# Performance work log

Measured on AMD Instinct MI355X. Metric: run time of the kernel, lower is better.

## Reference

```python
import jax, jax.numpy as jnp
import numpy as np

CONTEXT_FRAMES = 10
H = 200  # LSTM hidden size
F = 48   # tactile feature size
A = 6    # action dim


def _lstm_cell(x, h, c, Wih, Whh, bih, bhh):
    # PyTorch gate order: i, f, g, o
    gates = x @ Wih.T + h @ Whh.T + (bih + bhh)
    i, f, g, o = jnp.split(gates, 4, axis=-1)
    i = jax.nn.sigmoid(i)
    f = jax.nn.sigmoid(f)
    g = jnp.tanh(g)
    o = jax.nn.sigmoid(o)
    c = f * c + i * g
    h = o * jnp.tanh(c)
    return h, c


def setup_inputs() -> dict:
    key = jax.random.key(0)
    ks = jax.random.split(key, 16)
    T, B = 120, 4096
    tactiles = jax.random.normal(ks[0], (T, B, F), dtype=jnp.float32)
    actions = jax.random.normal(ks[1], (T, B, A), dtype=jnp.float32)
    s = 1.0 / np.sqrt(H)
    u = lambda k, shp: jax.random.uniform(k, shp, jnp.float32, -s, s)
    return {
        "tactiles": tactiles,
        "actions": actions,
        # lstm1: input 48 -> hidden 200
        "W_ih1": u(ks[2], (4 * H, F)), "W_hh1": u(ks[3], (4 * H, H)),
        "b_ih1": u(ks[4], (4 * H,)), "b_hh1": u(ks[5], (4 * H,)),
        # lstm2: input 248 -> hidden 200
        "W_ih2": u(ks[6], (4 * H, H + F)), "W_hh2": u(ks[7], (4 * H, H)),
        "b_ih2": u(ks[8], (4 * H,)), "b_hh2": u(ks[9], (4 * H,)),
        # fc1: 248 -> 200, fc2: 200 -> 48
        "fc1_w": u(ks[10], (H, H + F)), "fc1_b": u(ks[11], (H,)),
        "fc2_w": u(ks[12], (F, H)), "fc2_b": u(ks[13], (F,)),
    }


def reference(tactiles, actions, W_ih1, W_hh1, b_ih1, b_hh1,
              W_ih2, W_hh2, b_ih2, b_hh2, fc1_w, fc1_b, fc2_w, fc2_b):
    T, B, _ = tactiles.shape
    state = actions[0]  # [B, A]

    def step(carry, xs):
        h1, c1, h2, c2, prev_out4 = carry
        tact_t, act_t, t = xs
        # after the context window, feed back the previous prediction
        inp = jnp.where(t > CONTEXT_FRAMES - 1, prev_out4, tact_t)  # [B, 48]
        h1, c1 = _lstm_cell(inp, h1, c1, W_ih1, W_hh1, b_ih1, b_hh1)
        tiled = jnp.tile(jnp.concatenate([act_t, state], axis=1), (1, 4))  # [B, 48]
        x2 = jnp.concatenate([h1, tiled], axis=1)  # [B, 248]
        h2, c2 = _lstm_cell(x2, h2, c2, W_ih2, W_hh2, b_ih2, b_hh2)
        x3 = jnp.concatenate([h2, inp], axis=1)  # [B, 248]
        out3 = jnp.tanh(x3 @ fc1_w.T + fc1_b)
        out4 = jnp.tanh(out3 @ fc2_w.T + fc2_b)  # [B, 48]
        return (h1, c1, h2, c2, out4), out4

    z = lambda d: jnp.zeros((B, d), dtype=tactiles.dtype)
    carry0 = (z(H), z(H), z(H), z(H), z(F))
    xs = (tactiles[:-1], actions[1:], jnp.arange(T - 1))
    _, out4s = jax.lax.scan(step, carry0, xs)
    # torch code returns [last context out4] + [out4 for index 10..T-2]
    return out4s[CONTEXT_FRAMES - 1:]  # [T - 10, B, 48]
```

## Files before the change

### kernel.cpp

```cpp
#include <hip/hip_runtime.h>
#include <stdint.h>
#include <stddef.h>

#define HDIM 200
#define FDIM 48
#define ADIM 6
#define BTOT 4096
#define NSTEP 119
#define CTXM1 9
#define MROWS 16

typedef __attribute__((ext_vector_type(8))) short short8;
typedef __attribute__((ext_vector_type(4))) float floatx4;

#define OFF_W1P 0u
#define OFF_W2P 425984u
#define OFF_W3P 1171456u
#define OFF_W4P 1277952u
#define OFF_B1  1299456u
#define OFF_B2  1302784u
#define OFF_B3  1306112u
#define OFF_B4  1306944u

__device__ __forceinline__ unsigned short f2bf(float f) {
  unsigned int u = __float_as_uint(f);
  u += 0x7FFFu + ((u >> 16) & 1u);
  return (unsigned short)(u >> 16);
}
__device__ __forceinline__ float sigm(float x) {
  return 1.0f / (1.0f + __expf(-x));
}
__device__ __forceinline__ float tanh_(float x) {
  return 1.0f - 2.0f / (1.0f + __expf(2.0f * x));
}

__global__ void actp_pack(
    const float* __restrict__ Wih1, const float* __restrict__ Whh1,
    const float* __restrict__ bih1, const float* __restrict__ bhh1,
    const float* __restrict__ Wih2, const float* __restrict__ Whh2,
    const float* __restrict__ bih2, const float* __restrict__ bhh2,
    const float* __restrict__ fc1w, const float* __restrict__ fc1b,
    const float* __restrict__ fc2w, const float* __restrict__ fc2b,
    unsigned short* __restrict__ W1p, unsigned short* __restrict__ W2p,
    unsigned short* __restrict__ W3p, unsigned short* __restrict__ W4p,
    float* __restrict__ b1, float* __restrict__ b2,
    float* __restrict__ b3, float* __restrict__ b4) {
  int g = blockIdx.x * blockDim.x + threadIdx.x;
  if (g < 26624) {
    int lane = g & 63, tc = g >> 6;
    int chunk = tc & 7, tile = tc >> 3;
    int p = tile * 16 + (lane & 15);
    int gate = p / 208, u = p - gate * 208;
    int srow = gate * 200 + u;
    int kb = chunk * 32 + (lane >> 4) * 8;
    unsigned short* d = W1p + (size_t)g * 8;
#pragma unroll
    for (int j = 0; j < 8; ++j) {
      int k = kb + j;
      float v = 0.f;
      if (u < 200) {
        if (k < 48) v = Wih1[srow * 48 + k];
        else if (k < 248) v = Whh1[srow * 200 + (k - 48)];
      }
      d[j] = f2bf(v);
    }
  } else if (g < 73216) {
    int g2 = g - 26624;
    int lane = g2 & 63, tc = g2 >> 6;
    int chunk = tc % 14, tile = tc / 14;
    int p = tile * 16 + (lane & 15);
    int gate = p / 208, u = p - gate * 208;
    int srow = gate * 200 + u;
    int kb = chunk * 32 + (lane >> 4) * 8;
    unsigned short* d = W2p + (size_t)g2 * 8;
#pragma unroll
    for (int j = 0; j < 8; ++j) {
      int k = kb + j;
      float v = 0.f;
      if (u < 200) v = (k < 248) ? Wih2[srow * 248 + k] : Whh2[srow * 200 + (k - 248)];
      d[j] = f2bf(v);
    }
  } else if (g < 79872) {
    int g3 = g - 73216;
    int lane = g3 & 63, tc = g3 >> 6;
    int chunk = tc & 7, tile = tc >> 3;
    int p = tile * 16 + (lane & 15);
    int kb = chunk * 32 + (lane >> 4) * 8;
    unsigned short* d = W3p + (size_t)g3 * 8;
#pragma unroll
    for (int j = 0; j < 8; ++j) {
      int k = kb + j;
      float v = (p < 200 && k < 248) ? fc1w[p * 248 + k] : 0.f;
      d[j] = f2bf(v);
    }
  } else if (g < 81216) {
    int g4 = g - 79872;
    int lane = g4 & 63, tc = g4 >> 6;
    int chunk = tc % 7, tile = tc / 7;
    int p = tile * 16 + (lane & 15);
    int kb = chunk * 32 + (lane >> 4) * 8;
    unsigned short* d = W4p + (size_t)g4 * 8;
#pragma unroll
    for (int j = 0; j < 8; ++j) {
      int k = kb + j;
      float v = (k < 200) ? fc2w[p * 200 + k] : 0.f;
      d[j] = f2bf(v);
    }
  } else if (g < 81216 + 1920) {
    int i = g - 81216;
    if (i < 832) {
      int gate = i / 208, u = i - gate * 208;
      b1[i] = (u < 200) ? (bih1[gate * 200 + u] + bhh1[gate * 200 + u]) : 0.f;
    } else if (i < 1664) {
      int p = i - 832;
      int gate = p / 208, u = p - gate * 208;
      b2[p] = (u < 200) ? (bih2[gate * 200 + u] + bhh2[gate * 200 + u]) : 0.f;
    } else if (i < 1872) {
      int p = i - 1664;
      b3[p] = (p < 200) ? fc1b[p] : 0.f;
    } else {
      int p = i - 1872;
      b4[p] = fc2b[p];
    }
  }
}

__global__ __launch_bounds__(512, 2) void actp_main(
    const float* __restrict__ tact,
    const float* __restrict__ acts,
    const unsigned short* __restrict__ W1p, const unsigned short* __restrict__ W2p,
    const unsigned short* __restrict__ W3p, const unsigned short* __restrict__ W4p,
    const float* __restrict__ b1, const float* __restrict__ b2,
    const float* __restrict__ b3, const float* __restrict__ b4,
    float* __restrict__ out)
{
  __shared__ unsigned short x1[2][MROWS][264];
  __shared__ unsigned short x2[2][MROWS][456];
  __shared__ unsigned short x3[MROWS][264];
  __shared__ unsigned short x4[MROWS][232];
  __shared__ float c1s[MROWS][228];
  __shared__ float c2s[MROWS][228];

  const int tid = threadIdx.x;
  const int wv = tid >> 6;
  const int lane = tid & 63;
  const int n16 = lane & 15;
  const int qd = lane >> 4;
  const int row0 = (int)blockIdx.x * MROWS;

  for (int i = tid; i < 2 * MROWS * 264; i += 512) (&x1[0][0][0])[i] = 0;
  for (int i = tid; i < 2 * MROWS * 456; i += 512) (&x2[0][0][0])[i] = 0;
  for (int i = tid; i < MROWS * 264; i += 512) (&x3[0][0])[i] = 0;
  for (int i = tid; i < MROWS * 232; i += 512) (&x4[0][0])[i] = 0;
  for (int i = tid; i < MROWS * 228; i += 512) { (&c1s[0][0])[i] = 0.f; (&c2s[0][0])[i] = 0.f; }
  if (tid < 192) {
    int r = tid / 12, f0 = (tid % 12) * 4;
    const float* src = &tact[((size_t)(row0 + r)) * FDIM + f0];
#pragma unroll
    for (int j = 0; j < 4; ++j) {
      unsigned short v = f2bf(src[j]);
      x1[0][r][f0 + j] = v;
      x3[r][HDIM + f0 + j] = v;
    }
  } else if (tid < 384) {
    int idx = tid - 192;
    int r = idx / 12, a = idx % 12;
    float vf = (a < ADIM) ? acts[((size_t)BTOT + row0 + r) * ADIM + a]
                          : acts[((size_t)(row0 + r)) * ADIM + (a - ADIM)];
    unsigned short v = f2bf(vf);
    unsigned short* d = &x2[0][r][HDIM];
    d[a] = v; d[12 + a] = v; d[24 + a] = v; d[36 + a] = v;
  }
  __syncthreads();

  for (int t = 0; t < NSTEP; ++t) {
    const int cur = t & 1, nxt = cur ^ 1;

    {
      short8 A0[8];
#pragma unroll
      for (int c = 0; c < 8; ++c) A0[c] = *(const short8*)&x1[cur][n16][c * 32 + qd * 8];
      for (int ut = wv; ut < 13; ut += 8) {
        float bi = b1[(0 * 13 + ut) * 16 + n16];
        float bff = b1[(1 * 13 + ut) * 16 + n16];
        float bg = b1[(2 * 13 + ut) * 16 + n16];
        float bo = b1[(3 * 13 + ut) * 16 + n16];
        floatx4 ai = {bi, bi, bi, bi}, af = {bff, bff, bff, bff};
        floatx4 ag = {bg, bg, bg, bg}, ao = {bo, bo, bo, bo};
        const short8* wi = (const short8*)W1p + (size_t)(0 * 13 + ut) * 8 * 64 + lane;
        const short8* wf = (const short8*)W1p + (size_t)(1 * 13 + ut) * 8 * 64 + lane;
        const short8* wg = (const short8*)W1p + (size_t)(2 * 13 + ut) * 8 * 64 + lane;
        const short8* wo = (const short8*)W1p + (size_t)(3 * 13 + ut) * 8 * 64 + lane;
#pragma unroll
        for (int c = 0; c < 8; ++c) {
          ai = __builtin_amdgcn_mfma_f32_16x16x32_bf16(A0[c], wi[c * 64], ai, 0, 0, 0);
          af = __builtin_amdgcn_mfma_f32_16x16x32_bf16(A0[c], wf[c * 64], af, 0, 0, 0);
          ag = __builtin_amdgcn_mfma_f32_16x16x32_bf16(A0[c], wg[c * 64], ag, 0, 0, 0);
          ao = __builtin_amdgcn_mfma_f32_16x16x32_bf16(A0[c], wo[c * 64], ao, 0, 0, 0);
        }
        int u = ut * 16 + n16;
        bool live = (u < HDIM);
#pragma unroll
        for (int r = 0; r < 4; ++r) {
          int m = qd * 4 + r;
          float gi = sigm(ai[r]), gf = sigm(af[r]);
          float gg = tanh_(ag[r]), go = sigm(ao[r]);
          float cp = c1s[m][u];
          float cn = gf * cp + gi * gg;
          float hn = go * tanh_(cn);
          if (live) {
            c1s[m][u] = cn;
            unsigned short hb = f2bf(hn);
            x2[cur][m][u] = hb;
            x1[nxt][m][FDIM + u] = hb;
          }
        }
      }
    }
    __syncthreads();

    {
      short8 A0[14];
#pragma unroll
      for (int c = 0; c < 14; ++c) A0[c] = *(const short8*)&x2[cur][n16][c * 32 + qd * 8];
      for (int ut = wv; ut < 13; ut += 8) {
        float bi = b2[(0 * 13 + ut) * 16 + n16];
        float bff = b2[(1 * 13 + ut) * 16 + n16];
        float bg = b2[(2 * 13 + ut) * 16 + n16];
        float bo = b2[(3 * 13 + ut) * 16 + n16];
        floatx4 ai = {bi, bi, bi, bi}, af = {bff, bff, bff, bff};
        floatx4 ag = {bg, bg, bg, bg}, ao = {bo, bo, bo, bo};
        const short8* wi = (const short8*)W2p + (size_t)(0 * 13 + ut) * 14 * 64 + lane;
        const short8* wf = (const short8*)W2p + (size_t)(1 * 13 + ut) * 14 * 64 + lane;
        const short8* wg = (const short8*)W2p + (size_t)(2 * 13 + ut) * 14 * 64 + lane;
        const short8* wo = (const short8*)W2p + (size_t)(3 * 13 + ut) * 14 * 64 + lane;
#pragma unroll
        for (int c = 0; c < 14; ++c) {
          ai = __builtin_amdgcn_mfma_f32_16x16x32_bf16(A0[c], wi[c * 64], ai, 0, 0, 0);
          af = __builtin_amdgcn_mfma_f32_16x16x32_bf16(A0[c], wf[c * 64], af, 0, 0, 0);
          ag = __builtin_amdgcn_mfma_f32_16x16x32_bf16(A0[c], wg[c * 64], ag, 0, 0, 0);
          ao = __builtin_amdgcn_mfma_f32_16x16x32_bf16(A0[c], wo[c * 64], ao, 0, 0, 0);
        }
        int u = ut * 16 + n16;
        bool live = (u < HDIM);
#pragma unroll
        for (int r = 0; r < 4; ++r) {
          int m = qd * 4 + r;
          float gi = sigm(ai[r]), gf = sigm(af[r]);
          float gg = tanh_(ag[r]), go = sigm(ao[r]);
          float cp = c2s[m][u];
          float cn = gf * cp + gi * gg;
          float hn = go * tanh_(cn);
          if (live) {
            c2s[m][u] = cn;
            unsigned short hb = f2bf(hn);
            x3[m][u] = hb;
            x2[nxt][m][248 + u] = hb;
          }
        }
      }
    }
    __syncthreads();

    if (t >= CTXM1) {
      {
        short8 A0[8];
#pragma unroll
        for (int c = 0; c < 8; ++c) A0[c] = *(const short8*)&x3[n16][c * 32 + qd * 8];
        for (int nt = wv; nt < 13; nt += 8) {
          float bb = b3[nt * 16 + n16];
          floatx4 ac = {bb, bb, bb, bb};
          const short8* wp = (const short8*)W3p + (size_t)nt * 8 * 64 + lane;
#pragma unroll
          for (int c = 0; c < 8; ++c)
            ac = __builtin_amdgcn_mfma_f32_16x16x32_bf16(A0[c], wp[c * 64], ac, 0, 0, 0);
          int col = nt * 16 + n16;
#pragma unroll
          for (int r = 0; r < 4; ++r) x4[qd * 4 + r][col] = f2bf(tanh_(ac[r]));
        }
      }
      __syncthreads();
      if (wv < 3) {
        short8 A0[7];
#pragma unroll
        for (int c = 0; c < 7; ++c) A0[c] = *(const short8*)&x4[n16][c * 32 + qd * 8];
        float bb = b4[wv * 16 + n16];
        floatx4 ac = {bb, bb, bb, bb};
        const short8* wp = (const short8*)W4p + (size_t)wv * 7 * 64 + lane;
#pragma unroll
        for (int c = 0; c < 7; ++c)
          ac = __builtin_amdgcn_mfma_f32_16x16x32_bf16(A0[c], wp[c * 64], ac, 0, 0, 0);
        int col = wv * 16 + n16;
#pragma unroll
        for (int r = 0; r < 4; ++r) {
          int m = qd * 4 + r;
          float of = tanh_(ac[r]);
          out[((size_t)(t - CTXM1) * BTOT + row0 + m) * FDIM + col] = of;
          if (t < NSTEP - 1) {
            unsigned short bv = f2bf(of);
            x1[nxt][m][col] = bv;
            x3[m][HDIM + col] = bv;
          }
        }
      }
    } else {
      if (wv < 3) {
        int idx = wv * 64 + lane;
        int r = idx / 12, f0 = (idx % 12) * 4;
        const float* src = &tact[((size_t)(t + 1) * BTOT + row0 + r) * FDIM + f0];
#pragma unroll
        for (int j = 0; j < 4; ++j) {
          unsigned short v = f2bf(src[j]);
          x1[nxt][r][f0 + j] = v;
          x3[r][HDIM + f0 + j] = v;
        }
      }
    }
    if (wv >= 3 && wv < 6 && t < NSTEP - 1) {
      int idx = (wv - 3) * 64 + lane;
      int r = idx / 12, a = idx % 12;
      float vf = (a < ADIM) ? acts[((size_t)(t + 2) * BTOT + row0 + r) * ADIM + a]
                            : acts[((size_t)(row0 + r)) * ADIM + (a - ADIM)];
      unsigned short v = f2bf(vf);
      unsigned short* d = &x2[nxt][r][HDIM];
      d[a] = v; d[12 + a] = v; d[24 + a] = v; d[36 + a] = v;
    }
    __syncthreads();
  }
}

extern "C" void kernel_launch(void* const* d_in, const int* in_sizes, int n_in,
                              void* d_out, int out_size, void* d_ws, size_t ws_size,
                              hipStream_t stream) {
  const float* tact = (const float*)d_in[0];
  const float* acts = (const float*)d_in[1];
  const float* Wih1 = (const float*)d_in[2];
  const float* Whh1 = (const float*)d_in[3];
  const float* bih1 = (const float*)d_in[4];
  const float* bhh1 = (const float*)d_in[5];
  const float* Wih2 = (const float*)d_in[6];
  const float* Whh2 = (const float*)d_in[7];
  const float* bih2 = (const float*)d_in[8];
  const float* bhh2 = (const float*)d_in[9];
  const float* fc1w = (const float*)d_in[10];
  const float* fc1b = (const float*)d_in[11];
  const float* fc2w = (const float*)d_in[12];
  const float* fc2b = (const float*)d_in[13];

  uint8_t* ws = (uint8_t*)d_ws;
  unsigned short* W1p = (unsigned short*)(ws + OFF_W1P);
  unsigned short* W2p = (unsigned short*)(ws + OFF_W2P);
  unsigned short* W3p = (unsigned short*)(ws + OFF_W3P);
  unsigned short* W4p = (unsigned short*)(ws + OFF_W4P);
  float* b1 = (float*)(ws + OFF_B1);
  float* b2 = (float*)(ws + OFF_B2);
  float* b3 = (float*)(ws + OFF_B3);
  float* b4 = (float*)(ws + OFF_B4);

  hipLaunchKernelGGL(actp_pack, dim3(325), dim3(256), 0, stream,
                     Wih1, Whh1, bih1, bhh1, Wih2, Whh2, bih2, bhh2,
                     fc1w, fc1b, fc2w, fc2b, W1p, W2p, W3p, W4p, b1, b2, b3, b4);
  hipLaunchKernelGGL(actp_main, dim3(256), dim3(512), 0, stream,
                     tact, acts, W1p, W2p, W3p, W4p, b1, b2, b3, b4,
                     (float*)d_out);
}
```

Measured before the change: 2.065 ms.

## Use 16 waves per block with one gate tile per wave and dedicated loader waves

The block grows from 512 to 1024 threads. Each of 13 waves now computes exactly one 16-column gate tile, where before 8 waves looped over 13 tiles and needed two rounds. Three spare waves prefetch the next step's actions and tactile inputs while the LSTM1 phase runs. Bias values and weight pointers are hoisted out of the time loop, and `__syncthreads` is replaced by an inline-asm `s_waitcnt lgkmcnt(0)` plus `s_barrier`. The aim is to shorten the serial critical path of each recurrent step. In exchange, `launch_bounds(1024,4)` caps registers per thread, which risks spilling the 14-entry A fragment arrays.

```diff
diff --git a/kernel.cpp b/kernel.cpp
--- a/kernel.cpp
+++ b/kernel.cpp
@@ -12,6 +12,8 @@
 
 typedef __attribute__((ext_vector_type(8))) short short8;
 typedef __attribute__((ext_vector_type(4))) float floatx4;
+
+#define SOFTBAR() asm volatile("s_waitcnt lgkmcnt(0)\n\ts_barrier" ::: "memory")
 
 #define OFF_W1P 0u
 #define OFF_W2P 425984u
@@ -27,12 +29,8 @@
   u += 0x7FFFu + ((u >> 16) & 1u);
   return (unsigned short)(u >> 16);
 }
-__device__ __forceinline__ float sigm(float x) {
-  return 1.0f / (1.0f + __expf(-x));
-}
-__device__ __forceinline__ float tanh_(float x) {
-  return 1.0f - 2.0f / (1.0f + __expf(2.0f * x));
-}
+__device__ __forceinline__ float sigm(float x) { return 1.0f / (1.0f + __expf(-x)); }
+__device__ __forceinline__ float tanh_(float x) { return 1.0f - 2.0f / (1.0f + __expf(2.0f * x)); }
 
 __global__ void actp_pack(
     const float* __restrict__ Wih1, const float* __restrict__ Whh1,
@@ -106,7 +104,7 @@
       float v = (k < 200) ? fc2w[p * 200 + k] : 0.f;
       d[j] = f2bf(v);
     }
-  } else if (g < 81216 + 1920) {
+  } else if (g < 83136) {
     int i = g - 81216;
     if (i < 832) {
       int gate = i / 208, u = i - gate * 208;
@@ -125,7 +123,7 @@
   }
 }
 
-__global__ __launch_bounds__(512, 2) void actp_main(
+__global__ __launch_bounds__(1024, 4) void actp_main(
     const float* __restrict__ tact,
     const float* __restrict__ acts,
     const unsigned short* __restrict__ W1p, const unsigned short* __restrict__ W2p,
@@ -148,11 +146,30 @@
   const int qd = lane >> 4;
   const int row0 = (int)blockIdx.x * MROWS;
 
-  for (int i = tid; i < 2 * MROWS * 264; i += 512) (&x1[0][0][0])[i] = 0;
-  for (int i = tid; i < 2 * MROWS * 456; i += 512) (&x2[0][0][0])[i] = 0;
-  for (int i = tid; i < MROWS * 264; i += 512) (&x3[0][0])[i] = 0;
-  for (int i = tid; i < MROWS * 232; i += 512) (&x4[0][0])[i] = 0;
-  for (int i = tid; i < MROWS * 228; i += 512) { (&c1s[0][0])[i] = 0.f; (&c2s[0][0])[i] = 0.f; }
+  const int uw = (wv < 13) ? wv : 0;
+  float b1g[4], b2g[4];
+#pragma unroll
+  for (int g = 0; g < 4; ++g) {
+    b1g[g] = b1[(g * 13 + uw) * 16 + n16];
+    b2g[g] = b2[(g * 13 + uw) * 16 + n16];
+  }
+  const float b3s = b3[uw * 16 + n16];
+  const float b4s = b4[((wv < 3) ? wv : 0) * 16 + n16];
+  const short8* w1b[4];
+  const short8* w2b[4];
+#pragma unroll
+  for (int g = 0; g < 4; ++g) {
+    w1b[g] = (const short8*)W1p + (size_t)(g * 13 + uw) * 8 * 64 + lane;
+    w2b[g] = (const short8*)W2p + (size_t)(g * 13 + uw) * 14 * 64 + lane;
+  }
+  const short8* w3p = (const short8*)W3p + (size_t)uw * 8 * 64 + lane;
+  const short8* w4p = (const short8*)W4p + (size_t)((wv < 3) ? wv : 0) * 7 * 64 + lane;
+
+  for (int i = tid; i < 2 * MROWS * 264; i += 1024) (&x1[0][0][0])[i] = 0;
+  for (int i = tid; i < 2 * MROWS * 456; i += 1024) (&x2[0][0][0])[i] = 0;
+  for (int i = tid; i < MROWS * 264; i += 1024) (&x3[0][0])[i] = 0;
+  for (int i = tid; i < MROWS * 232; i += 1024) (&x4[0][0])[i] = 0;
+  for (int i = tid; i < MROWS * 228; i += 1024) { (&c1s[0][0])[i] = 0.f; (&c2s[0][0])[i] = 0.f; }
   if (tid < 192) {
     int r = tid / 12, f0 = (tid % 12) * 4;
     const float* src = &tact[((size_t)(row0 + r)) * FDIM + f0];
@@ -176,120 +193,122 @@
   for (int t = 0; t < NSTEP; ++t) {
     const int cur = t & 1, nxt = cur ^ 1;
 
-    {
+    if (wv < 13) {
       short8 A0[8];
 #pragma unroll
       for (int c = 0; c < 8; ++c) A0[c] = *(const short8*)&x1[cur][n16][c * 32 + qd * 8];
-      for (int ut = wv; ut < 13; ut += 8) {
-        float bi = b1[(0 * 13 + ut) * 16 + n16];
-        float bff = b1[(1 * 13 + ut) * 16 + n16];
-        float bg = b1[(2 * 13 + ut) * 16 + n16];
-        float bo = b1[(3 * 13 + ut) * 16 + n16];
-        floatx4 ai = {bi, bi, bi, bi}, af = {bff, bff, bff, bff};
-        floatx4 ag = {bg, bg, bg, bg}, ao = {bo, bo, bo, bo};
-        const short8* wi = (const short8*)W1p + (size_t)(0 * 13 + ut) * 8 * 64 + lane;
-        const short8* wf = (const short8*)W1p + (size_t)(1 * 13 + ut) * 8 * 64 + lane;
-        const short8* wg = (const short8*)W1p + (size_t)(2 * 13 + ut) * 8 * 64 + lane;
-        const short8* wo = (const short8*)W1p + (size_t)(3 * 13 + ut) * 8 * 64 + lane;
-#pragma unroll
-        for (int c = 0; c < 8; ++c) {
-          ai = __builtin_amdgcn_mfma_f32_16x16x32_bf16(A0[c], wi[c * 64], ai, 0, 0, 0);
-          af = __builtin_amdgcn_mfma_f32_16x16x32_bf16(A0[c], wf[c * 64], af, 0, 0, 0);
-          ag = __builtin_amdgcn_mfma_f32_16x16x32_bf16(A0[c], wg[c * 64], ag, 0, 0, 0);
-          ao = __builtin_amdgcn_mfma_f32_16x16x32_bf16(A0[c], wo[c * 64], ao, 0, 0, 0);
-        }
-        int u = ut * 16 + n16;
-        bool live = (u < HDIM);
-#pragma unroll
-        for (int r = 0; r < 4; ++r) {
-          int m = qd * 4 + r;
-          float gi = sigm(ai[r]), gf = sigm(af[r]);
-          float gg = tanh_(ag[r]), go = sigm(ao[r]);
-          float cp = c1s[m][u];
-          float cn = gf * cp + gi * gg;
-          float hn = go * tanh_(cn);
-          if (live) {
-            c1s[m][u] = cn;
-            unsigned short hb = f2bf(hn);
-            x2[cur][m][u] = hb;
-            x1[nxt][m][FDIM + u] = hb;
+      floatx4 ai = {b1g[0], b1g[0], b1g[0], b1g[0]};
+      floatx4 af = {b1g[1], b1g[1], b1g[1], b1g[1]};
+      floatx4 ag = {b1g[2], b1g[2], b1g[2], b1g[2]};
+      floatx4 ao = {b1g[3], b1g[3], b1g[3], b1g[3]};
+#pragma unroll
+      for (int c = 0; c < 8; ++c) {
+        ai = __builtin_amdgcn_mfma_f32_16x16x32_bf16(A0[c], w1b[0][c * 64], ai, 0, 0, 0);
+        af = __builtin_amdgcn_mfma_f32_16x16x32_bf16(A0[c], w1b[1][c * 64], af, 0, 0, 0);
+        ag = __builtin_amdgcn_mfma_f32_16x16x32_bf16(A0[c], w1b[2][c * 64], ag, 0, 0, 0);
+        ao = __builtin_amdgcn_mfma_f32_16x16x32_bf16(A0[c], w1b[3][c * 64], ao, 0, 0, 0);
+      }
+      int u = wv * 16 + n16;
+      bool live = (u < HDIM);
+#pragma unroll
+      for (int r = 0; r < 4; ++r) {
+        int m = qd * 4 + r;
+        float gi = sigm(ai[r]), gf = sigm(af[r]);
+        float gg = tanh_(ag[r]), go = sigm(ao[r]);
+        float cp = c1s[m][u];
+        float cn = gf * cp + gi * gg;
+        float hn = go * tanh_(cn);
+        if (live) {
+          c1s[m][u] = cn;
+          unsigned short hb = f2bf(hn);
+          x2[cur][m][u] = hb;
+          x1[nxt][m][FDIM + u] = hb;
+        }
+      }
+    } else if (wv == 13) {
+      if (t < NSTEP - 1) {
+        for (int i = lane; i < MROWS * 12; i += 64) {
+          int r = i / 12, a = i % 12;
+          float vf = (a < ADIM) ? acts[((size_t)(t + 2) * BTOT + row0 + r) * ADIM + a]
+                                : acts[((size_t)(row0 + r)) * ADIM + (a - ADIM)];
+          unsigned short v = f2bf(vf);
+          unsigned short* d = &x2[nxt][r][HDIM];
+          d[a] = v; d[12 + a] = v; d[24 + a] = v; d[36 + a] = v;
+        }
+      }
+    } else {
+      if (t < CTXM1) {
+        for (int i = (wv - 14) * 64 + lane; i < MROWS * 12; i += 128) {
+          int r = i / 12, f0 = (i % 12) * 4;
+          const float* src = &tact[((size_t)(t + 1) * BTOT + row0 + r) * FDIM + f0];
+#pragma unroll
+          for (int j = 0; j < 4; ++j) {
+            unsigned short v = f2bf(src[j]);
+            x1[nxt][r][f0 + j] = v;
+            x3[r][HDIM + f0 + j] = v;
           }
         }
       }
     }
-    __syncthreads();
-
-    {
+    SOFTBAR();
+
+    if (wv < 13) {
       short8 A0[14];
 #pragma unroll
       for (int c = 0; c < 14; ++c) A0[c] = *(const short8*)&x2[cur][n16][c * 32 + qd * 8];
-      for (int ut = wv; ut < 13; ut += 8) {
-        float bi = b2[(0 * 13 + ut) * 16 + n16];
-        float bff = b2[(1 * 13 + ut) * 16 + n16];
-        float bg = b2[(2 * 13 + ut) * 16 + n16];
-        float bo = b2[(3 * 13 + ut) * 16 + n16];
-        floatx4 ai = {bi, bi, bi, bi}, af = {bff, bff, bff, bff};
-        floatx4 ag = {bg, bg, bg, bg}, ao = {bo, bo, bo, bo};
-        const short8* wi = (const short8*)W2p + (size_t)(0 * 13 + ut) * 14 * 64 + lane;
-        const short8* wf = (const short8*)W2p + (size_t)(1 * 13 + ut) * 14 * 64 + lane;
-        const short8* wg = (const short8*)W2p + (size_t)(2 * 13 + ut) * 14 * 64 + lane;
-        const short8* wo = (const short8*)W2p + (size_t)(3 * 13 + ut) * 14 * 64 + lane;
-#pragma unroll
-        for (int c = 0; c < 14; ++c) {
-          ai = __builtin_amdgcn_mfma_f32_16x16x32_bf16(A0[c], wi[c * 64], ai, 0, 0, 0);
-          af = __builtin_amdgcn_mfma_f32_16x16x32_bf16(A0[c], wf[c * 64], af, 0, 0, 0);
-          ag = __builtin_amdgcn_mfma_f32_16x16x32_bf16(A0[c], wg[c * 64], ag, 0, 0, 0);
-          ao = __builtin_amdgcn_mfma_f32_16x16x32_bf16(A0[c], wo[c * 64], ao, 0, 0, 0);
-        }
-        int u = ut * 16 + n16;
-        bool live = (u < HDIM);
-#pragma unroll
-        for (int r = 0; r < 4; ++r) {
-          int m = qd * 4 + r;
-          float gi = sigm(ai[r]), gf = sigm(af[r]);
-          float gg = tanh_(ag[r]), go = sigm(ao[r]);
-          float cp = c2s[m][u];
-          float cn = gf * cp + gi * gg;
-          float hn = go * tanh_(cn);
-          if (live) {
-            c2s[m][u] = cn;
-            unsigned short hb = f2bf(hn);
-            x3[m][u] = hb;
-            x2[nxt][m][248 + u] = hb;
-          }
-        }
-      }
-    }
-    __syncthreads();
+      floatx4 ai = {b2g[0], b2g[0], b2g[0], b2g[0]};
+      floatx4 af = {b2g[1], b2g[1], b2g[1], b2g[1]};
+      floatx4 ag = {b2g[2], b2g[2], b2g[2], b2g[2]};
+      floatx4 ao = {b2g[3], b2g[3], b2g[3], b2g[3]};
+#pragma unroll
+      for (int c = 0; c < 14; ++c) {
+        ai = __builtin_amdgcn_mfma_f32_16x16x32_bf16(A0[c], w2b[0][c * 64], ai, 0, 0, 0);
+        af = __builtin_amdgcn_mfma_f32_16x16x32_bf16(A0[c], w2b[1][c * 64], af, 0, 0, 0);
+        ag = __builtin_amdgcn_mfma_f32_16x16x32_bf16(A0[c], w2b[2][c * 64], ag, 0, 0, 0);
+        ao = __builtin_amdgcn_mfma_f32_16x16x32_bf16(A0[c], w2b[3][c * 64], ao, 0, 0, 0);
+      }
+      int u = wv * 16 + n16;
+      bool live = (u < HDIM);
+#pragma unroll
+      for (int r = 0; r < 4; ++r) {
+        int m = qd * 4 + r;
+        float gi = sigm(ai[r]), gf = sigm(af[r]);
+        float gg = tanh_(ag[r]), go = sigm(ao[r]);
+        float cp = c2s[m][u];
+        float cn = gf * cp + gi * gg;
+        float hn = go * tanh_(cn);
+        if (live) {
+          c2s[m][u] = cn;
+          unsigned short hb = f2bf(hn);
+          x3[m][u] = hb;
+          x2[nxt][m][248 + u] = hb;
+        }
+      }
+    }
+    SOFTBAR();
 
     if (t >= CTXM1) {
-      {
+      if (wv < 13) {
         short8 A0[8];
 #pragma unroll
         for (int c = 0; c < 8; ++c) A0[c] = *(const short8*)&x3[n16][c * 32 + qd * 8];
-        for (int nt = wv; nt < 13; nt += 8) {
-          float bb = b3[nt * 16 + n16];
-          floatx4 ac = {bb, bb, bb, bb};
-          const short8* wp = (const short8*)W3p + (size_t)nt * 8 * 64 + lane;
-#pragma unroll
-          for (int c = 0; c < 8; ++c)
-            ac = __builtin_amdgcn_mfma_f32_16x16x32_bf16(A0[c], wp[c * 64], ac, 0, 0, 0);
-          int col = nt * 16 + n16;
-#pragma unroll
-          for (int r = 0; r < 4; ++r) x4[qd * 4 + r][col] = f2bf(tanh_(ac[r]));
-        }
-      }
-      __syncthreads();
+        floatx4 ac = {b3s, b3s, b3s, b3s};
+#pragma unroll
+        for (int c = 0; c < 8; ++c)
+          ac = __builtin_amdgcn_mfma_f32_16x16x32_bf16(A0[c], w3p[c * 64], ac, 0, 0, 0);
+        int col = wv * 16 + n16;
+#pragma unroll
+        for (int r = 0; r < 4; ++r) x4[qd * 4 + r][col] = f2bf(tanh_(ac[r]));
+      }
+      SOFTBAR();
       if (wv < 3) {
         short8 A0[7];
 #pragma unroll
         for (int c = 0; c < 7; ++c) A0[c] = *(const short8*)&x4[n16][c * 32 + qd * 8];
-        float bb = b4[wv * 16 + n16];
-        floatx4 ac = {bb, bb, bb, bb};
-        const short8* wp = (const short8*)W4p + (size_t)wv * 7 * 64 + lane;
+        floatx4 ac = {b4s, b4s, b4s, b4s};
 #pragma unroll
         for (int c = 0; c < 7; ++c)
-          ac = __builtin_amdgcn_mfma_f32_16x16x32_bf16(A0[c], wp[c * 64], ac, 0, 0, 0);
+          ac = __builtin_amdgcn_mfma_f32_16x16x32_bf16(A0[c], w4p[c * 64], ac, 0, 0, 0);
         int col = wv * 16 + n16;
 #pragma unroll
         for (int r = 0; r < 4; ++r) {
@@ -303,29 +322,8 @@
           }
         }
       }
-    } else {
-      if (wv < 3) {
-        int idx = wv * 64 + lane;
-        int r = idx / 12, f0 = (idx % 12) * 4;
-        const float* src = &tact[((size_t)(t + 1) * BTOT + row0 + r) * FDIM + f0];
-#pragma unroll
-        for (int j = 0; j < 4; ++j) {
-          unsigned short v = f2bf(src[j]);
-          x1[nxt][r][f0 + j] = v;
-          x3[r][HDIM + f0 + j] = v;
-        }
-      }
-    }
-    if (wv >= 3 && wv < 6 && t < NSTEP - 1) {
-      int idx = (wv - 3) * 64 + lane;
-      int r = idx / 12, a = idx % 12;
-      float vf = (a < ADIM) ? acts[((size_t)(t + 2) * BTOT + row0 + r) * ADIM + a]
-                            : acts[((size_t)(row0 + r)) * ADIM + (a - ADIM)];
-      unsigned short v = f2bf(vf);
-      unsigned short* d = &x2[nxt][r][HDIM];
-      d[a] = v; d[12 + a] = v; d[24 + a] = v; d[36 + a] = v;
-    }
-    __syncthreads();
+    }
+    SOFTBAR();
   }
 }
 
@@ -360,7 +358,7 @@
   hipLaunchKernelGGL(actp_pack, dim3(325), dim3(256), 0, stream,
                      Wih1, Whh1, bih1, bhh1, Wih2, Whh2, bih2, bhh2,
                      fc1w, fc1b, fc2w, fc2b, W1p, W2p, W3p, W4p, b1, b2, b3, b4);
-  hipLaunchKernelGGL(actp_main, dim3(256), dim3(512), 0, stream,
+  hipLaunchKernelGGL(actp_main, dim3(256), dim3(1024), 0, stream,
                      tact, acts, W1p, W2p, W3p, W4p, b1, b2, b3, b4,
                      (float*)d_out);
 }
```

New measurement: 4.144 ms. 2.01x slower.
